# Performance work log

Measured on AMD Instinct MI355X. Metric: run time of the kernel, lower is better.

Reference implementation:

```python
import jax, jax.numpy as jnp
import numpy as np

T, TINI, N, P, M, B = 1500, 16, 32, 4, 4, 8192
LG = T - TINI - N + 1  # g dimension = 1453


def block_hankel(w, L, d):
    # w: flat signal of length T*d (row-major (T,d)); returns (L*d, T-L+1) block Hankel
    Tlen = w.shape[0] // d
    cols = Tlen - L + 1
    idx = jnp.arange(L * d)[:, None] + d * jnp.arange(cols)[None, :]
    return w[idx]


def setup_inputs():
    key = jax.random.key(0)
    ks = jax.random.split(key, 8)
    ud = jax.random.normal(ks[0], (T, M), jnp.float32)
    yd = jax.random.normal(ks[1], (T, P), jnp.float32)
    q = 100.0 + 0.01 * jax.random.normal(ks[2], (P,), jnp.float32)   # torch init: randn*0.01+100
    r = 0.01 + 0.001 * jax.random.normal(ks[3], (M,), jnp.float32)   # torch init: randn*0.001+0.01
    ref = jax.random.normal(ks[4], (B, N * P), jnp.float32)
    uref = jnp.zeros((B, N * M), jnp.float32)  # unused by forward math (matches torch)
    u_ini = jax.random.normal(ks[5], (B, TINI * M), jnp.float32)
    y_ini = jax.random.normal(ks[6], (B, TINI * P), jnp.float32)
    return dict(ref=ref, uref=uref, u_ini=u_ini, y_ini=y_ini, ud=ud, yd=yd, q=q, r=r)


def _forward(ref, u_ini, y_ini, ud, yd, q, r):
    # Hankel data matrices
    U = block_hankel(ud.reshape(-1), TINI + N, M)   # (M*(TINI+N), LG)
    Y = block_hankel(yd.reshape(-1), TINI + N, P)
    Up, Uf = U[: M * TINI], U[M * TINI :]           # (M*TINI, LG), (M*N, LG)
    Yp, Yf = Y[: P * TINI], Y[P * TINI :]

    # cost weights: Q_sqrt = diag(kron(ones(N), sqrt(q))) => squared weights tile(q, N)
    wq = jnp.tile(q, N)  # (N*P,)
    wr = jnp.tile(r, N)  # (N*M,)

    # QP in g: min g^T H g - 2 (Yf^T Wq ref)^T g  s.t.  A g = b
    H = Yf.T @ (wq[:, None] * Yf) + Uf.T @ (wr[:, None] * Uf)  # (LG, LG)
    A = jnp.concatenate([Up, Yp, Yf[-P:]], axis=0)             # equality constraints: Up g=u_ini, Yp g=y_ini, y[-P:]=ref[-P:]
    nc = A.shape[0]

    K = jnp.block([[2.0 * H, A.T], [A, jnp.zeros((nc, nc), H.dtype)]])  # KKT matrix (shared over batch)
    rhs = jnp.concatenate(
        [2.0 * (Yf.T @ (wq[:, None] * ref.T)), u_ini.T, y_ini.T, ref[:, -P:].T], axis=0
    )  # (LG+nc, B)

    sol = jnp.linalg.pinv(K) @ rhs   # min-norm KKT solution (K is singular: g non-unique, u/y unique)
    g = sol[:LG].T                   # (B, LG)
    u = g @ Uf.T                     # (B, N*M) optimal input
    y = g @ Yf.T                     # (B, N*P) optimal output
    return g, u, y


def reference(ref, uref, u_ini, y_ini, ud, yd, q, r):
    # uref is unused in the torch forward math as well (only a None-default placeholder)
    return _forward(ref, u_ini, y_ini, ud, yd, q, r)
```

## Files before the change

### kernel.cpp

```cpp
#include <hip/hip_runtime.h>

#define COLS_ 1453
#define NC 132
#define EGS 1792
#define NB 8192

#define oGam 0
#define oC   147456
#define oV   196608
#define oGC  213504
#define oCK  262656
#define oVK  311808
#define oGCK 328704
#define oB   377856
#define oP   410624
#define oR   414980
#define oJ   431364
#define oF   464132
#define oCE  496900

typedef short v8s __attribute__((ext_vector_type(8)));
typedef float v4f __attribute__((ext_vector_type(4)));

__device__ __forceinline__ double hash01(unsigned i, unsigned j) {
  unsigned x = i * 0x9E3779B9u ^ (j * 0x85EBCA6Bu + 0xC2B2AE35u);
  x ^= x >> 16; x *= 0x7FEB352Du; x ^= x >> 15; x *= 0x846CA68Bu; x ^= x >> 16;
  return (double)(x & 0xFFFFFF) / 8388608.0 - 1.0;
}

__device__ __forceinline__ unsigned short f2bf(float x) {
  union { float f; unsigned u; } v; v.f = x;
  unsigned r = (v.u + 0x7FFFu + ((v.u >> 16) & 1u)) >> 16;
  return (unsigned short)r;
}
__device__ __forceinline__ float bf2f(unsigned short h) {
  union { unsigned u; float f; } v; v.u = ((unsigned)h) << 16; return v.f;
}

__global__ void k_gram(const float* __restrict__ ud, const float* __restrict__ yd,
                       double* __restrict__ G) {
  __shared__ float sig[12000];
  int tid = threadIdx.y * 16 + threadIdx.x;
  for (int idx = tid; idx < 6000; idx += 256) { sig[idx] = ud[idx]; sig[6000 + idx] = yd[idx]; }
  __syncthreads();
  int i = blockIdx.y * 16 + threadIdx.y;
  int j = blockIdx.x * 16 + threadIdx.x;
  const float* si = &sig[(i < 192) ? i : (6000 + i - 192)];
  const float* sj = &sig[(j < 192) ? j : (6000 + j - 192)];
  double a0 = 0.0, a1 = 0.0, a2 = 0.0, a3 = 0.0;
  for (int c = 0; c < 1452; c += 4) {
    a0 += (double)si[4 * c]      * (double)sj[4 * c];
    a1 += (double)si[4 * c + 4]  * (double)sj[4 * c + 4];
    a2 += (double)si[4 * c + 8]  * (double)sj[4 * c + 8];
    a3 += (double)si[4 * c + 12] * (double)sj[4 * c + 12];
  }
  a0 += (double)si[4 * 1452] * (double)sj[4 * 1452];
  G[i * 384 + j] = (a0 + a1) + (a2 + a3);
}

__global__ void k_initc(double* __restrict__ c, double* __restrict__ v) {
  int z = blockIdx.x * 16 + threadIdx.x;
  int i = blockIdx.y * 16 + threadIdx.y;
  if (i < 384) c[i * 128 + z] = hash01(i, z);
  else if (i < 516) v[(i - 384) * 128 + z] = hash01(i + 1000, z);
}

__global__ void k_G(const double* __restrict__ Gam, const double* __restrict__ c,
                    double* __restrict__ outp) {
  int z = blockIdx.x * 16 + threadIdx.x;
  int i = blockIdx.y * 16 + threadIdx.y;
  double a0 = 0.0, a1 = 0.0;
  for (int t = 0; t < 384; t += 2) {
    a0 += Gam[i * 384 + t]     * c[t * 128 + z];
    a1 += Gam[i * 384 + t + 1] * c[(t + 1) * 128 + z];
  }
  outp[i * 128 + z] = a0 + a1;
}

__global__ void k_step(const double* __restrict__ GC, const double* __restrict__ v,
                       const float* __restrict__ q, const float* __restrict__ r,
                       double* __restrict__ cK, double* __restrict__ vK) {
  int z = blockIdx.x * 16 + threadIdx.x;
  int i = blockIdx.y * 16 + threadIdx.y;
  if (i >= 516) return;
  if (i < 384) {
    double val;
    if (i < 64)        val = v[i * 128 + z];
    else if (i < 192)  { int m = i - 64;  val = 2.0 * (double)r[m & 3] * GC[i * 128 + z]; }
    else if (i < 256)  val = v[(64 + i - 192) * 128 + z];
    else {
      int m = i - 256;
      val = 2.0 * (double)q[m & 3] * GC[i * 128 + z];
      if (m >= 124) val += v[(128 + m - 124) * 128 + z];
    }
    cK[i * 128 + z] = val;
  } else {
    int rr = i - 384;
    double val;
    if (rr < 64)       val = GC[rr * 128 + z];
    else if (rr < 128) val = GC[(192 + rr - 64) * 128 + z];
    else               val = GC[(380 + rr - 128) * 128 + z];
    vK[rr * 128 + z] = val;
  }
}

__global__ void k_normc(double* __restrict__ c, double* __restrict__ v, double* __restrict__ GC) {
  __shared__ double red[256];
  int z = blockIdx.x, tid = threadIdx.x;
  double s = 0.0;
  for (int i = tid; i < 384; i += 256) s += c[i * 128 + z] * GC[i * 128 + z];
  for (int rr = tid; rr < 132; rr += 256) { double t = v[rr * 128 + z]; s += t * t; }
  red[tid] = s; __syncthreads();
  for (int st = 128; st > 0; st >>= 1) { if (tid < st) red[tid] += red[tid + st]; __syncthreads(); }
  double inv = rsqrt(red[0]);
  for (int i = tid; i < 384; i += 256) { c[i * 128 + z] *= inv; GC[i * 128 + z] *= inv; }
  for (int rr = tid; rr < 132; rr += 256) v[rr * 128 + z] *= inv;
}

__global__ void k_B(const double* __restrict__ c, const double* __restrict__ GCK,
                    const double* __restrict__ v, const double* __restrict__ vK,
                    double* __restrict__ Baug) {
  int z2 = blockIdx.x * 16 + threadIdx.x;
  int z1 = blockIdx.y * 16 + threadIdx.y;
  if (z2 >= 128) { Baug[z1 * 256 + z2] = ((z2 - 128) == z1) ? 1.0 : 0.0; return; }
  double a0 = 0.0, a1 = 0.0;
  for (int i = 0; i < 384; i += 2) {
    a0 += c[i * 128 + z1] * GCK[i * 128 + z2];
    a1 += c[(i + 1) * 128 + z1] * GCK[(i + 1) * 128 + z2];
  }
  for (int rr = 0; rr < 132; ++rr) a0 += v[rr * 128 + z1] * vK[rr * 128 + z2];
  Baug[z1 * 256 + z2] = a0 + a1;
}

__global__ __launch_bounds__(512) void k_inv(const double* __restrict__ src, int srcStride,
                                             double* __restrict__ dst, int n) {
  (void)n;
  __shared__ double pr[2][64];
  __shared__ double ckb[2][64];
  const int tid = threadIdx.x;
  const int r  = tid >> 3;
  const int cg = tid & 7;
  double a[8];
#pragma unroll
  for (int jj = 0; jj < 8; ++jj) a[jj] = src[r * srcStride + jj * 8 + cg];
#pragma unroll 1
  for (int k = 0; k < 64; ++k) {
    const int par = k & 1;
    const int ke = k & 7;
    const int kj = k >> 3;
    if (r == k) {
#pragma unroll
      for (int jj = 0; jj < 8; ++jj) pr[par][jj * 8 + cg] = a[jj];
    }
    if (cg == ke) {
#pragma unroll
      for (int jj = 0; jj < 8; ++jj) if (jj == kj) ckb[par][r] = a[jj];
    }
    __syncthreads();
    double pv  = 1.0 / pr[par][k];
    double fik = ckb[par][r];
    bool  isk  = (r == k);
    double f   = fik * pv;
    double fp  = isk ? (1.0 - pv) : f;
#pragma unroll
    for (int jj = 0; jj < 8; ++jj) a[jj] -= fp * pr[par][jj * 8 + cg];
    if (cg == ke) {
#pragma unroll
      for (int jj = 0; jj < 8; ++jj) if (jj == kj) a[jj] = isk ? pv : -f;
    }
  }
#pragma unroll
  for (int jj = 0; jj < 8; ++jj) dst[r * 64 + jj * 8 + cg] = a[jj];
}

__global__ void k_rowscale(const double* __restrict__ Maug, const double* __restrict__ P,
                           double* __restrict__ R, int stride, int nb, int k) {
  int c = nb * (k + 1) + blockIdx.x * 64 + threadIdx.x;
  if (c >= stride) return;
  int rr = blockIdx.y;
  double acc = 0.0;
  for (int t = 0; t < nb; ++t) acc += P[rr * nb + t] * Maug[(nb * k + t) * stride + c];
  R[rr * stride + c] = acc;
}

__global__ void k_update(double* __restrict__ Maug, const double* __restrict__ R,
                         int stride, int n, int nb, int k) {
  int c = nb * (k + 1) + blockIdx.x * 64 + threadIdx.x;
  if (c >= stride) return;
  int i = blockIdx.y;
  int ib = i - nb * k;
  if (ib >= 0 && ib < nb) { Maug[i * stride + c] = R[ib * stride + c]; return; }
  double acc = Maug[i * stride + c];
  for (int t = 0; t < nb; ++t) acc -= Maug[i * stride + nb * k + t] * R[t * stride + c];
  Maug[i * stride + c] = acc;
}

__global__ void k_J(const double* __restrict__ GC, const double* __restrict__ v,
                    const float* __restrict__ q, double* __restrict__ J) {
  int t = blockIdx.x * 16 + threadIdx.x;
  int z = blockIdx.y * 16 + threadIdx.y;
  double val;
  if (t < 128) {
    val = 2.0 * (double)q[t & 3] * GC[(256 + t) * 128 + z];
    if (t >= 124) val += v[(128 + t - 124) * 128 + z];
  } else if (t < 192) {
    val = v[(t - 128) * 128 + z];
  } else {
    val = v[(64 + t - 192) * 128 + z];
  }
  J[z * 256 + t] = val;
}

__global__ void k_F(const double* __restrict__ Baug, const double* __restrict__ J,
                    double* __restrict__ F) {
  int t = blockIdx.x * 16 + threadIdx.x;
  int z = blockIdx.y * 16 + threadIdx.y;
  double a0 = 0.0, a1 = 0.0;
  for (int w = 0; w < 128; w += 2) {
    a0 += Baug[z * 256 + 128 + w] * J[w * 256 + t];
    a1 += Baug[z * 256 + 128 + w + 1] * J[(w + 1) * 256 + t];
  }
  F[z * 256 + t] = a0 + a1;
}

__global__ void k_CE(const double* __restrict__ c, const double* __restrict__ F,
                     double* __restrict__ CEt) {
  int i = blockIdx.x * 16 + threadIdx.x;
  int t = blockIdx.y * 16 + threadIdx.y;
  double a0 = 0.0, a1 = 0.0;
  for (int z = 0; z < 128; z += 2) {
    a0 += c[i * 128 + z] * F[z * 256 + t];
    a1 += c[i * 128 + z + 1] * F[(z + 1) * 256 + t];
  }
  CEt[t * 384 + i] = a0 + a1;
}

__global__ void k_Egt(const double* __restrict__ CEt, const float* __restrict__ ud,
                      const float* __restrict__ yd, unsigned short* __restrict__ Eh,
                      unsigned short* __restrict__ El) {
  __shared__ float sig[12000];
  int tid = threadIdx.y * 16 + threadIdx.x;
  for (int idx = tid; idx < 6000; idx += 256) { sig[idx] = ud[idx]; sig[6000 + idx] = yd[idx]; }
  __syncthreads();
  int c = blockIdx.x * 16 + threadIdx.x;
  int t = blockIdx.y * 16 + threadIdx.y;
  double a0 = 0.0, a1 = 0.0, a2 = 0.0, a3 = 0.0;
  if (c < COLS_) {
    const double* ce = &CEt[(size_t)t * 384];
    const float*  su = &sig[4 * c];
    const float*  sy = &sig[6000 + 4 * c];
#pragma unroll 4
    for (int i0 = 0; i0 < 192; i0 += 8) {
      float4 s0 = *(const float4*)&su[i0];
      float4 s1 = *(const float4*)&su[i0 + 4];
      double2 c0 = *(const double2*)&ce[i0];
      double2 c1 = *(const double2*)&ce[i0 + 2];
      double2 c2 = *(const double2*)&ce[i0 + 4];
      double2 c3 = *(const double2*)&ce[i0 + 6];
      a0 += c0.x * (double)s0.x;  a1 += c0.y * (double)s0.y;
      a2 += c1.x * (double)s0.z;  a3 += c1.y * (double)s0.w;
      a0 += c2.x * (double)s1.x;  a1 += c2.y * (double)s1.y;
      a2 += c3.x * (double)s1.z;  a3 += c3.y * (double)s1.w;
    }
    const double* cey = ce + 192;
#pragma unroll 4
    for (int i0 = 0; i0 < 192; i0 += 8) {
      float4 s0 = *(const float4*)&sy[i0];
      float4 s1 = *(const float4*)&sy[i0 + 4];
      double2 c0 = *(const double2*)&cey[i0];
      double2 c1 = *(const double2*)&cey[i0 + 2];
      double2 c2 = *(const double2*)&cey[i0 + 4];
      double2 c3 = *(const double2*)&cey[i0 + 6];
      a0 += c0.x * (double)s0.x;  a1 += c0.y * (double)s0.y;
      a2 += c1.x * (double)s0.z;  a3 += c1.y * (double)s0.w;
      a0 += c2.x * (double)s1.x;  a1 += c2.y * (double)s1.y;
      a2 += c3.x * (double)s1.z;  a3 += c3.y * (double)s1.w;
    }
  }
  double s = (a0 + a1) + (a2 + a3);
  float f = (float)s;
  unsigned short h = f2bf(f);
  float lo = (float)(s - (double)bf2f(h));
  Eh[t * EGS + c] = h;
  El[t * EGS + c] = f2bf(lo);
}

__global__ void k_Euy(const double* __restrict__ GC, const double* __restrict__ F,
                      unsigned short* __restrict__ Eh, unsigned short* __restrict__ El) {
  int n = blockIdx.x * 16 + threadIdx.x;
  int t = blockIdx.y * 16 + threadIdx.y;
  int row = (n < 128) ? (64 + n) : (128 + n);
  double a0 = 0.0, a1 = 0.0;
  for (int z = 0; z < 128; z += 2) {
    a0 += GC[row * 128 + z] * F[z * 256 + t];
    a1 += GC[row * 128 + z + 1] * F[(z + 1) * 256 + t];
  }
  double s = a0 + a1;
  float f = (float)s;
  unsigned short h = f2bf(f);
  float lo = (float)(s - (double)bf2f(h));
  Eh[t * EGS + 1536 + n] = h;
  El[t * EGS + 1536 + n] = f2bf(lo);
}

__device__ __forceinline__ float4 loadA4(const float* __restrict__ ref, const float* __restrict__ ui,
                                         const float* __restrict__ yi, int m, int j) {
  if (j < 128) return *(const float4*)&ref[m * 128 + j];
  if (j < 192) return *(const float4*)&ui[m * 64 + (j - 128)];
  return *(const float4*)&yi[m * 64 + (j - 192)];
}

__global__ __launch_bounds__(256, 2) void k_gemm1(const float* __restrict__ ref, const float* __restrict__ ui,
                                                  const float* __restrict__ yi,
                                                  const unsigned short* __restrict__ Eh,
                                                  const unsigned short* __restrict__ El,
                                                  float* __restrict__ gout, float* __restrict__ uout,
                                                  float* __restrict__ yout) {
  __shared__ unsigned short Ah[128 * 32];
  __shared__ unsigned short Al[128 * 32];
  __shared__ unsigned short Bh[128 * 32];
  __shared__ unsigned short Bl[128 * 32];
  const int tid = threadIdx.x;
  const int m0 = blockIdx.y * 128;
  const int n0 = blockIdx.x * 128;
  const int w  = tid >> 6;
  const int lane = tid & 63;
  const int wm = (w >> 1) * 64;
  const int wn = (w & 1) * 64;
  const int fr = lane & 15;
  const int kg = lane >> 4;
  const int sRow = tid & 127;
  const int sKh  = tid >> 7;
  const int sXor = (sRow >> 1) & 3;

  v4f acc[4][4];
#pragma unroll
  for (int i = 0; i < 4; ++i)
#pragma unroll
    for (int j = 0; j < 4; ++j) acc[i][j] = (v4f){0.0f, 0.0f, 0.0f, 0.0f};

  float4 q0, q1, q2, q3;
  unsigned short eh[16], el[16];

  {
    const int jb = sKh * 16;
    q0 = loadA4(ref, ui, yi, m0 + sRow, jb + 0);
    q1 = loadA4(ref, ui, yi, m0 + sRow, jb + 4);
    q2 = loadA4(ref, ui, yi, m0 + sRow, jb + 8);
    q3 = loadA4(ref, ui, yi, m0 + sRow, jb + 12);
#pragma unroll
    for (int e = 0; e < 16; ++e) {
      int idx = (jb + e) * EGS + n0 + sRow;
      eh[e] = Eh[idx];
      el[e] = El[idx];
    }
  }

  for (int k0 = 0; k0 < 256; k0 += 32) {
    float xa[16] = {q0.x, q0.y, q0.z, q0.w, q1.x, q1.y, q1.z, q1.w,
                    q2.x, q2.y, q2.z, q2.w, q3.x, q3.y, q3.z, q3.w};
    union { v8s s; unsigned u[4]; } ah0, ah1, al0, al1;
#pragma unroll
    for (int p = 0; p < 8; ++p) {
      float x0 = xa[2 * p], x1 = xa[2 * p + 1];
      unsigned hp, lp;
      asm("v_cvt_pk_bf16_f32 %0, %1, %2" : "=v"(hp) : "v"(x0), "v"(x1));
      union { unsigned u; float f; } h0, h1;
      h0.u = hp << 16;
      h1.u = hp & 0xFFFF0000u;
      float l0 = x0 - h0.f;
      float l1 = x1 - h1.f;
      asm("v_cvt_pk_bf16_f32 %0, %1, %2" : "=v"(lp) : "v"(l0), "v"(l1));
      if (p < 4) { ah0.u[p] = hp; al0.u[p] = lp; }
      else       { ah1.u[p - 4] = hp; al1.u[p - 4] = lp; }
    }
    v8s bh0, bh1, bl0, bl1;
#pragma unroll
    for (int e = 0; e < 8; ++e) {
      bh0[e] = (short)eh[e];
      bh1[e] = (short)eh[8 + e];
      bl0[e] = (short)el[e];
      bl1[e] = (short)el[8 + e];
    }
    __syncthreads();
    {
      const int s0 = ((sKh * 2 + 0) ^ sXor) * 8;
      const int s1 = ((sKh * 2 + 1) ^ sXor) * 8;
      *(v8s*)&Ah[sRow * 32 + s0] = ah0.s;
      *(v8s*)&Ah[sRow * 32 + s1] = ah1.s;
      *(v8s*)&Al[sRow * 32 + s0] = al0.s;
      *(v8s*)&Al[sRow * 32 + s1] = al1.s;
      *(v8s*)&Bh[sRow * 32 + s0] = bh0;
      *(v8s*)&Bh[sRow * 32 + s1] = bh1;
      *(v8s*)&Bl[sRow * 32 + s0] = bl0;
      *(v8s*)&Bl[sRow * 32 + s1] = bl1;
    }
    __syncthreads();
    if (k0 < 224) {
      const int jb = k0 + 32 + sKh * 16;
      q0 = loadA4(ref, ui, yi, m0 + sRow, jb + 0);
      q1 = loadA4(ref, ui, yi, m0 + sRow, jb + 4);
      q2 = loadA4(ref, ui, yi, m0 + sRow, jb + 8);
      q3 = loadA4(ref, ui, yi, m0 + sRow, jb + 12);
#pragma unroll
      for (int e = 0; e < 16; ++e) {
        int idx = (jb + e) * EGS + n0 + sRow;
        eh[e] = Eh[idx];
        el[e] = El[idx];
      }
    }
    v8s fah[4], fal[4], fbh[4], fbl[4];
#pragma unroll
    for (int t4 = 0; t4 < 4; ++t4) {
      int ar = wm + t4 * 16 + fr;
      int as = (kg ^ ((ar >> 1) & 3)) * 8;
      fah[t4] = *(const v8s*)&Ah[ar * 32 + as];
      fal[t4] = *(const v8s*)&Al[ar * 32 + as];
      int bc = wn + t4 * 16 + fr;
      int bs = (kg ^ ((bc >> 1) & 3)) * 8;
      fbh[t4] = *(const v8s*)&Bh[bc * 32 + bs];
      fbl[t4] = *(const v8s*)&Bl[bc * 32 + bs];
    }
#pragma unroll
    for (int tm = 0; tm < 4; ++tm)
#pragma unroll
      for (int tn = 0; tn < 4; ++tn) {
        acc[tm][tn] = __builtin_amdgcn_mfma_f32_16x16x32_bf16(fal[tm], fbh[tn], acc[tm][tn], 0, 0, 0);
        acc[tm][tn] = __builtin_amdgcn_mfma_f32_16x16x32_bf16(fah[tm], fbl[tn], acc[tm][tn], 0, 0, 0);
        acc[tm][tn] = __builtin_amdgcn_mfma_f32_16x16x32_bf16(fah[tm], fbh[tn], acc[tm][tn], 0, 0, 0);
      }
  }
#pragma unroll
  for (int tm = 0; tm < 4; ++tm) {
    const int mb = m0 + wm + tm * 16 + kg * 4;
#pragma unroll
    for (int tn = 0; tn < 4; ++tn) {
      const int n = n0 + wn + tn * 16 + fr;
#pragma unroll
      for (int r = 0; r < 4; ++r) {
        float vv = acc[tm][tn][r];
        int m = mb + r;
        if (n < COLS_)       gout[(size_t)m * COLS_ + n] = vv;
        else if (n >= 1664)  yout[m * 128 + (n - 1664)] = vv;
        else if (n >= 1536)  uout[m * 128 + (n - 1536)] = vv;
      }
    }
  }
}

extern "C" void kernel_launch(void* const* d_in, const int* in_sizes, int n_in,
                              void* d_out, int out_size, void* d_ws, size_t ws_size,
                              hipStream_t stream) {
  (void)in_sizes; (void)n_in; (void)out_size; (void)ws_size;
  const float* ref   = (const float*)d_in[0];
  const float* u_ini = (const float*)d_in[2];
  const float* y_ini = (const float*)d_in[3];
  const float* ud    = (const float*)d_in[4];
  const float* yd    = (const float*)d_in[5];
  const float* q     = (const float*)d_in[6];
  const float* r     = (const float*)d_in[7];

  float* out  = (float*)d_out;
  float* gout = out;
  float* uout = out + (size_t)NB * COLS_;
  float* yout = uout + (size_t)NB * 128;

  double* Wd  = (double*)d_out;
  double* Gam = Wd + oGam;
  double* c   = Wd + oC;
  double* v   = Wd + oV;
  double* GC  = Wd + oGC;
  double* cK  = Wd + oCK;
  double* vK  = Wd + oVK;
  double* GCK = Wd + oGCK;
  double* Ba  = Wd + oB;
  double* P   = Wd + oP;
  double* R   = Wd + oR;
  double* J   = Wd + oJ;
  double* F   = Wd + oF;
  double* CEt = Wd + oCE;
  unsigned short* Eh = (unsigned short*)d_ws;
  unsigned short* El = Eh + (size_t)256 * EGS;

  k_gram<<<dim3(24, 24), dim3(16, 16), 0, stream>>>(ud, yd, Gam);

  k_initc<<<dim3(8, 33), dim3(16, 16), 0, stream>>>(c, v);
  double* ca = c;  double* va = v;
  double* cb = cK; double* vb = vK;
  for (int it = 0; it < 4; ++it) {
    k_G<<<dim3(8, 24), dim3(16, 16), 0, stream>>>(Gam, ca, GC);
    k_step<<<dim3(8, 33), dim3(16, 16), 0, stream>>>(GC, va, q, r, cb, vb);
    double* t1 = ca; ca = cb; cb = t1;
    double* t2 = va; va = vb; vb = t2;
  }

  k_G<<<dim3(8, 24), dim3(16, 16), 0, stream>>>(Gam, ca, GC);
  k_normc<<<128, 256, 0, stream>>>(ca, va, GC);
  k_step<<<dim3(8, 33), dim3(16, 16), 0, stream>>>(GC, va, q, r, cb, vb);
  k_G<<<dim3(8, 24), dim3(16, 16), 0, stream>>>(Gam, cb, GCK);
  k_B<<<dim3(16, 8), dim3(16, 16), 0, stream>>>(ca, GCK, va, vb, Ba);

  for (int k = 0; k < 2; ++k) {
    k_inv<<<1, 512, 0, stream>>>(Ba + (size_t)(64 * k) * 256 + 64 * k, 256, P, 64);
    int cs = 64 * (k + 1);
    int gx = (256 - cs + 63) / 64;
    k_rowscale<<<dim3(gx, 64), 64, 0, stream>>>(Ba, P, R, 256, 64, k);
    k_update<<<dim3(gx, 128), 64, 0, stream>>>(Ba, R, 256, 64, 64, k);
  }

  k_J<<<dim3(16, 8), dim3(16, 16), 0, stream>>>(GC, va, q, J);
  k_F<<<dim3(16, 8), dim3(16, 16), 0, stream>>>(Ba, J, F);
  k_CE<<<dim3(24, 16), dim3(16, 16), 0, stream>>>(ca, F, CEt);
  k_Egt<<<dim3(96, 16), dim3(16, 16), 0, stream>>>(CEt, ud, yd, Eh, El);
  k_Euy<<<dim3(16, 16), dim3(16, 16), 0, stream>>>(GC, F, Eh, El);

  k_gemm1<<<dim3(14, 64), dim3(256), 0, stream>>>(ref, u_ini, y_ini, Eh, El, gout, uout, yout);
}
```

Before: 555.6 us.

## Transpose E storage and load MFMA fragments directly from global, dropping LDS staging

The E matrices are now written k-contiguous per output column, so each lane in the final GEMM can load its 8-element bf16 fragment straight from global memory. The A operand is also read per-fragment from global and split into hi/lo in registers. This removes shared-memory staging and both block barriers per k-step. The cost is redundant global/L2 reads across waves sharing rows or columns, plus higher register use now that the occupancy hint is dropped. Writes of E in k_Egt become strided, with t as the inner index.

```diff
diff --git a/kernel.cpp b/kernel.cpp
--- a/kernel.cpp
+++ b/kernel.cpp
@@ -2,7 +2,6 @@
 
 #define COLS_ 1453
 #define NC 132
-#define EGS 1792
 #define NB 8192
 
 #define oGam 0
@@ -236,8 +235,8 @@
 }
 
 __global__ void k_Egt(const double* __restrict__ CEt, const float* __restrict__ ud,
-                      const float* __restrict__ yd, unsigned short* __restrict__ Eh,
-                      unsigned short* __restrict__ El) {
+                      const float* __restrict__ yd, unsigned short* __restrict__ Eht,
+                      unsigned short* __restrict__ Elt) {
   __shared__ float sig[12000];
   int tid = threadIdx.y * 16 + threadIdx.x;
   for (int idx = tid; idx < 6000; idx += 256) { sig[idx] = ud[idx]; sig[6000 + idx] = yd[idx]; }
@@ -281,12 +280,12 @@
   float f = (float)s;
   unsigned short h = f2bf(f);
   float lo = (float)(s - (double)bf2f(h));
-  Eh[t * EGS + c] = h;
-  El[t * EGS + c] = f2bf(lo);
+  Eht[(size_t)c * 256 + t] = h;
+  Elt[(size_t)c * 256 + t] = f2bf(lo);
 }
 
 __global__ void k_Euy(const double* __restrict__ GC, const double* __restrict__ F,
-                      unsigned short* __restrict__ Eh, unsigned short* __restrict__ El) {
+                      unsigned short* __restrict__ Eht, unsigned short* __restrict__ Elt) {
   int n = blockIdx.x * 16 + threadIdx.x;
   int t = blockIdx.y * 16 + threadIdx.y;
   int row = (n < 128) ? (64 + n) : (128 + n);
@@ -299,8 +298,8 @@
   float f = (float)s;
   unsigned short h = f2bf(f);
   float lo = (float)(s - (double)bf2f(h));
-  Eh[t * EGS + 1536 + n] = h;
-  El[t * EGS + 1536 + n] = f2bf(lo);
+  Eht[(size_t)(1536 + n) * 256 + t] = h;
+  Elt[(size_t)(1536 + n) * 256 + t] = f2bf(lo);
 }
 
 __device__ __forceinline__ float4 loadA4(const float* __restrict__ ref, const float* __restrict__ ui,
@@ -310,16 +309,12 @@
   return *(const float4*)&yi[m * 64 + (j - 192)];
 }
 
-__global__ __launch_bounds__(256, 2) void k_gemm1(const float* __restrict__ ref, const float* __restrict__ ui,
-                                                  const float* __restrict__ yi,
-                                                  const unsigned short* __restrict__ Eh,
-                                                  const unsigned short* __restrict__ El,
-                                                  float* __restrict__ gout, float* __restrict__ uout,
-                                                  float* __restrict__ yout) {
-  __shared__ unsigned short Ah[128 * 32];
-  __shared__ unsigned short Al[128 * 32];
-  __shared__ unsigned short Bh[128 * 32];
-  __shared__ unsigned short Bl[128 * 32];
+__global__ __launch_bounds__(256) void k_gemm1(const float* __restrict__ ref, const float* __restrict__ ui,
+                                               const float* __restrict__ yi,
+                                               const unsigned short* __restrict__ Eht,
+                                               const unsigned short* __restrict__ Elt,
+                                               float* __restrict__ gout, float* __restrict__ uout,
+                                               float* __restrict__ yout) {
   const int tid = threadIdx.x;
   const int m0 = blockIdx.y * 128;
   const int n0 = blockIdx.x * 128;
@@ -329,9 +324,13 @@
   const int wn = (w & 1) * 64;
   const int fr = lane & 15;
   const int kg = lane >> 4;
-  const int sRow = tid & 127;
-  const int sKh  = tid >> 7;
-  const int sXor = (sRow >> 1) & 3;
+
+  int arow[4], bcol[4];
+#pragma unroll
+  for (int t4 = 0; t4 < 4; ++t4) {
+    arow[t4] = m0 + wm + t4 * 16 + fr;
+    bcol[t4] = n0 + wn + t4 * 16 + fr;
+  }
 
   v4f acc[4][4];
 #pragma unroll
@@ -339,87 +338,53 @@
 #pragma unroll
     for (int j = 0; j < 4; ++j) acc[i][j] = (v4f){0.0f, 0.0f, 0.0f, 0.0f};
 
-  float4 q0, q1, q2, q3;
-  unsigned short eh[16], el[16];
+  float4 pa0[4], pa1[4];
+  v8s pbh[4], pbl[4];
 
   {
-    const int jb = sKh * 16;
-    q0 = loadA4(ref, ui, yi, m0 + sRow, jb + 0);
-    q1 = loadA4(ref, ui, yi, m0 + sRow, jb + 4);
-    q2 = loadA4(ref, ui, yi, m0 + sRow, jb + 8);
-    q3 = loadA4(ref, ui, yi, m0 + sRow, jb + 12);
-#pragma unroll
-    for (int e = 0; e < 16; ++e) {
-      int idx = (jb + e) * EGS + n0 + sRow;
-      eh[e] = Eh[idx];
-      el[e] = El[idx];
-    }
-  }
-
+    const int kb = kg * 8;
+#pragma unroll
+    for (int t4 = 0; t4 < 4; ++t4) {
+      pa0[t4] = loadA4(ref, ui, yi, arow[t4], kb);
+      pa1[t4] = loadA4(ref, ui, yi, arow[t4], kb + 4);
+      pbh[t4] = *(const v8s*)&Eht[(size_t)bcol[t4] * 256 + kb];
+      pbl[t4] = *(const v8s*)&Elt[(size_t)bcol[t4] * 256 + kb];
+    }
+  }
+
+#pragma unroll
   for (int k0 = 0; k0 < 256; k0 += 32) {
-    float xa[16] = {q0.x, q0.y, q0.z, q0.w, q1.x, q1.y, q1.z, q1.w,
-                    q2.x, q2.y, q2.z, q2.w, q3.x, q3.y, q3.z, q3.w};
-    union { v8s s; unsigned u[4]; } ah0, ah1, al0, al1;
-#pragma unroll
-    for (int p = 0; p < 8; ++p) {
-      float x0 = xa[2 * p], x1 = xa[2 * p + 1];
-      unsigned hp, lp;
-      asm("v_cvt_pk_bf16_f32 %0, %1, %2" : "=v"(hp) : "v"(x0), "v"(x1));
-      union { unsigned u; float f; } h0, h1;
-      h0.u = hp << 16;
-      h1.u = hp & 0xFFFF0000u;
-      float l0 = x0 - h0.f;
-      float l1 = x1 - h1.f;
-      asm("v_cvt_pk_bf16_f32 %0, %1, %2" : "=v"(lp) : "v"(l0), "v"(l1));
-      if (p < 4) { ah0.u[p] = hp; al0.u[p] = lp; }
-      else       { ah1.u[p - 4] = hp; al1.u[p - 4] = lp; }
-    }
-    v8s bh0, bh1, bl0, bl1;
-#pragma unroll
-    for (int e = 0; e < 8; ++e) {
-      bh0[e] = (short)eh[e];
-      bh1[e] = (short)eh[8 + e];
-      bl0[e] = (short)el[e];
-      bl1[e] = (short)el[8 + e];
-    }
-    __syncthreads();
-    {
-      const int s0 = ((sKh * 2 + 0) ^ sXor) * 8;
-      const int s1 = ((sKh * 2 + 1) ^ sXor) * 8;
-      *(v8s*)&Ah[sRow * 32 + s0] = ah0.s;
-      *(v8s*)&Ah[sRow * 32 + s1] = ah1.s;
-      *(v8s*)&Al[sRow * 32 + s0] = al0.s;
-      *(v8s*)&Al[sRow * 32 + s1] = al1.s;
-      *(v8s*)&Bh[sRow * 32 + s0] = bh0;
-      *(v8s*)&Bh[sRow * 32 + s1] = bh1;
-      *(v8s*)&Bl[sRow * 32 + s0] = bl0;
-      *(v8s*)&Bl[sRow * 32 + s1] = bl1;
-    }
-    __syncthreads();
+    v8s fah[4], fal[4], fbh[4], fbl[4];
+#pragma unroll
+    for (int t4 = 0; t4 < 4; ++t4) {
+      float xa[8] = {pa0[t4].x, pa0[t4].y, pa0[t4].z, pa0[t4].w,
+                     pa1[t4].x, pa1[t4].y, pa1[t4].z, pa1[t4].w};
+      union { v8s s; unsigned u[4]; } hh, ll;
+#pragma unroll
+      for (int p = 0; p < 4; ++p) {
+        float x0 = xa[2 * p], x1 = xa[2 * p + 1];
+        unsigned hp, lp;
+        asm("v_cvt_pk_bf16_f32 %0, %1, %2" : "=v"(hp) : "v"(x0), "v"(x1));
+        union { unsigned u; float f; } h0, h1;
+        h0.u = hp << 16;
+        h1.u = hp & 0xFFFF0000u;
+        float l0 = x0 - h0.f;
+        float l1 = x1 - h1.f;
+        asm("v_cvt_pk_bf16_f32 %0, %1, %2" : "=v"(lp) : "v"(l0), "v"(l1));
+        hh.u[p] = hp; ll.u[p] = lp;
+      }
+      fah[t4] = hh.s; fal[t4] = ll.s;
+      fbh[t4] = pbh[t4]; fbl[t4] = pbl[t4];
+    }
     if (k0 < 224) {
-      const int jb = k0 + 32 + sKh * 16;
-      q0 = loadA4(ref, ui, yi, m0 + sRow, jb + 0);
-      q1 = loadA4(ref, ui, yi, m0 + sRow, jb + 4);
-      q2 = loadA4(ref, ui, yi, m0 + sRow, jb + 8);
-      q3 = loadA4(ref, ui, yi, m0 + sRow, jb + 12);
-#pragma unroll
-      for (int e = 0; e < 16; ++e) {
-        int idx = (jb + e) * EGS + n0 + sRow;
-        eh[e] = Eh[idx];
-        el[e] = El[idx];
+      const int kb = k0 + 32 + kg * 8;
+#pragma unroll
+      for (int t4 = 0; t4 < 4; ++t4) {
+        pa0[t4] = loadA4(ref, ui, yi, arow[t4], kb);
+        pa1[t4] = loadA4(ref, ui, yi, arow[t4], kb + 4);
+        pbh[t4] = *(const v8s*)&Eht[(size_t)bcol[t4] * 256 + kb];
+        pbl[t4] = *(const v8s*)&Elt[(size_t)bcol[t4] * 256 + kb];
       }
-    }
-    v8s fah[4], fal[4], fbh[4], fbl[4];
-#pragma unroll
-    for (int t4 = 0; t4 < 4; ++t4) {
-      int ar = wm + t4 * 16 + fr;
-      int as = (kg ^ ((ar >> 1) & 3)) * 8;
-      fah[t4] = *(const v8s*)&Ah[ar * 32 + as];
-      fal[t4] = *(const v8s*)&Al[ar * 32 + as];
-      int bc = wn + t4 * 16 + fr;
-      int bs = (kg ^ ((bc >> 1) & 3)) * 8;
-      fbh[t4] = *(const v8s*)&Bh[bc * 32 + bs];
-      fbl[t4] = *(const v8s*)&Bl[bc * 32 + bs];
     }
 #pragma unroll
     for (int tm = 0; tm < 4; ++tm)
@@ -479,8 +444,8 @@
   double* J   = Wd + oJ;
   double* F   = Wd + oF;
   double* CEt = Wd + oCE;
-  unsigned short* Eh = (unsigned short*)d_ws;
-  unsigned short* El = Eh + (size_t)256 * EGS;
+  unsigned short* Eht = (unsigned short*)d_ws;
+  unsigned short* Elt = Eht + (size_t)1792 * 256;
 
   k_gram<<<dim3(24, 24), dim3(16, 16), 0, stream>>>(ud, yd, Gam);
 
@@ -511,8 +476,8 @@
   k_J<<<dim3(16, 8), dim3(16, 16), 0, stream>>>(GC, va, q, J);
   k_F<<<dim3(16, 8), dim3(16, 16), 0, stream>>>(Ba, J, F);
   k_CE<<<dim3(24, 16), dim3(16, 16), 0, stream>>>(ca, F, CEt);
-  k_Egt<<<dim3(96, 16), dim3(16, 16), 0, stream>>>(CEt, ud, yd, Eh, El);
-  k_Euy<<<dim3(16, 16), dim3(16, 16), 0, stream>>>(GC, F, Eh, El);
-
-  k_gemm1<<<dim3(14, 64), dim3(256), 0, stream>>>(ref, u_ini, y_ini, Eh, El, gout, uout, yout);
-}
+  k_Egt<<<dim3(96, 16), dim3(16, 16), 0, stream>>>(CEt, ud, yd, Eht, Elt);
+  k_Euy<<<dim3(16, 16), dim3(16, 16), 0, stream>>>(GC, F, Eht, Elt);
+
+  k_gemm1<<<dim3(14, 64), dim3(256), 0, stream>>>(ref, u_ini, y_ini, Eht, Elt, gout, uout, yout);
+}
```

New measurement: 584.3 us. 5.2% more time.

## Replace blocked 128x128 inversion with single-kernel in-register Gauss-Jordan

Applied to the files above, without the earlier changes.

Swaps the two-step blocked inversion of the 128x128 matrix (64x64 inverse, row-scale, trailing-update kernels, six launches) for one 512-thread kernel that runs Gauss-Jordan in place over all 128 pivots. Each thread holds 32 doubles in registers, and the inverse is written straight into the right half of the augmented buffer. The aim is to remove launch overhead and intermediate global round trips. In exchange, the serial pivot loop doubles to 128 iterations, register pressure rises, and the 32-way select for the pivot column may compile to costly dynamic indexing.

```diff
diff --git a/kernel.cpp b/kernel.cpp
--- a/kernel.cpp
+++ b/kernel.cpp
@@ -132,29 +132,30 @@
   Baug[z1 * 256 + z2] = a0 + a1;
 }
 
-__global__ __launch_bounds__(512) void k_inv(const double* __restrict__ src, int srcStride,
-                                             double* __restrict__ dst, int n) {
-  (void)n;
-  __shared__ double pr[2][64];
-  __shared__ double ckb[2][64];
+__global__ __launch_bounds__(512) void k_inv128(double* __restrict__ Ba) {
+  __shared__ double pr[2][128];
+  __shared__ double ckb[2][128];
   const int tid = threadIdx.x;
-  const int r  = tid >> 3;
-  const int cg = tid & 7;
-  double a[8];
-#pragma unroll
-  for (int jj = 0; jj < 8; ++jj) a[jj] = src[r * srcStride + jj * 8 + cg];
+  const int r  = tid >> 2;
+  const int cg = tid & 3;
+  const int c0 = cg * 32;
+  double a[32];
+#pragma unroll
+  for (int jj = 0; jj < 32; ++jj) a[jj] = Ba[r * 256 + c0 + jj];
 #pragma unroll 1
-  for (int k = 0; k < 64; ++k) {
+  for (int k = 0; k < 128; ++k) {
     const int par = k & 1;
-    const int ke = k & 7;
-    const int kj = k >> 3;
+    const int ke = k >> 5;
+    const int kj = k & 31;
     if (r == k) {
 #pragma unroll
-      for (int jj = 0; jj < 8; ++jj) pr[par][jj * 8 + cg] = a[jj];
+      for (int jj = 0; jj < 32; ++jj) pr[par][c0 + jj] = a[jj];
     }
     if (cg == ke) {
-#pragma unroll
-      for (int jj = 0; jj < 8; ++jj) if (jj == kj) ckb[par][r] = a[jj];
+      double ck = a[0];
+#pragma unroll
+      for (int jj = 1; jj < 32; ++jj) ck = (jj == kj) ? a[jj] : ck;
+      ckb[par][r] = ck;
     }
     __syncthreads();
     double pv  = 1.0 / pr[par][k];
@@ -163,36 +164,15 @@
     double f   = fik * pv;
     double fp  = isk ? (1.0 - pv) : f;
 #pragma unroll
-    for (int jj = 0; jj < 8; ++jj) a[jj] -= fp * pr[par][jj * 8 + cg];
+    for (int jj = 0; jj < 32; ++jj) a[jj] -= fp * pr[par][c0 + jj];
     if (cg == ke) {
-#pragma unroll
-      for (int jj = 0; jj < 8; ++jj) if (jj == kj) a[jj] = isk ? pv : -f;
-    }
-  }
-#pragma unroll
-  for (int jj = 0; jj < 8; ++jj) dst[r * 64 + jj * 8 + cg] = a[jj];
-}
-
-__global__ void k_rowscale(const double* __restrict__ Maug, const double* __restrict__ P,
-                           double* __restrict__ R, int stride, int nb, int k) {
-  int c = nb * (k + 1) + blockIdx.x * 64 + threadIdx.x;
-  if (c >= stride) return;
-  int rr = blockIdx.y;
-  double acc = 0.0;
-  for (int t = 0; t < nb; ++t) acc += P[rr * nb + t] * Maug[(nb * k + t) * stride + c];
-  R[rr * stride + c] = acc;
-}
-
-__global__ void k_update(double* __restrict__ Maug, const double* __restrict__ R,
-                         int stride, int n, int nb, int k) {
-  int c = nb * (k + 1) + blockIdx.x * 64 + threadIdx.x;
-  if (c >= stride) return;
-  int i = blockIdx.y;
-  int ib = i - nb * k;
-  if (ib >= 0 && ib < nb) { Maug[i * stride + c] = R[ib * stride + c]; return; }
-  double acc = Maug[i * stride + c];
-  for (int t = 0; t < nb; ++t) acc -= Maug[i * stride + nb * k + t] * R[t * stride + c];
-  Maug[i * stride + c] = acc;
+      double nv = isk ? pv : -f;
+#pragma unroll
+      for (int jj = 0; jj < 32; ++jj) if (jj == kj) a[jj] = nv;
+    }
+  }
+#pragma unroll
+  for (int jj = 0; jj < 32; ++jj) Ba[r * 256 + 128 + c0 + jj] = a[jj];
 }
 
 __global__ void k_J(const double* __restrict__ GC, const double* __restrict__ v,
@@ -474,8 +454,6 @@
   double* vK  = Wd + oVK;
   double* GCK = Wd + oGCK;
   double* Ba  = Wd + oB;
-  double* P   = Wd + oP;
-  double* R   = Wd + oR;
   double* J   = Wd + oJ;
   double* F   = Wd + oF;
   double* CEt = Wd + oCE;
@@ -500,13 +478,7 @@
   k_G<<<dim3(8, 24), dim3(16, 16), 0, stream>>>(Gam, cb, GCK);
   k_B<<<dim3(16, 8), dim3(16, 16), 0, stream>>>(ca, GCK, va, vb, Ba);
 
-  for (int k = 0; k < 2; ++k) {
-    k_inv<<<1, 512, 0, stream>>>(Ba + (size_t)(64 * k) * 256 + 64 * k, 256, P, 64);
-    int cs = 64 * (k + 1);
-    int gx = (256 - cs + 63) / 64;
-    k_rowscale<<<dim3(gx, 64), 64, 0, stream>>>(Ba, P, R, 256, 64, k);
-    k_update<<<dim3(gx, 128), 64, 0, stream>>>(Ba, R, 256, 64, 64, k);
-  }
+  k_inv128<<<1, 512, 0, stream>>>(Ba);
 
   k_J<<<dim3(16, 8), dim3(16, 16), 0, stream>>>(GC, va, q, J);
   k_F<<<dim3(16, 8), dim3(16, 16), 0, stream>>>(Ba, J, F);
```

After: 793.5 us. 1.43x slower.
